# Optimization experiments

Measured on AMD Instinct MI355X. Metric: run time of the kernel, lower is better.

The kernel has to match this reference:

```python
import jax, jax.numpy as jnp
import numpy as np

DN = ('NCHW', 'OIHW', 'NCHW')


def dwconv(x, w, b, pad, dil=(1, 1)):
    # depthwise conv: w is (C, 1, kh, kw), feature_group_count = C
    y = jax.lax.conv_general_dilated(
        x, w, window_strides=(1, 1), padding=[pad[0], pad[1]],
        rhs_dilation=dil, dimension_numbers=DN, feature_group_count=w.shape[0])
    return y + b[None, :, None, None]


def setup_inputs() -> dict:
    key = jax.random.key(0)
    ks = jax.random.split(key, 18)
    dim, B, H, W = 512, 8, 64, 64
    s = 0.1  # keep depthwise chain numerically tame
    inp = {'x': jax.random.normal(ks[0], (B, dim, H, W), jnp.float32)}
    shapes = {
        'w0': (dim, 1, 5, 5), 'w0_1': (dim, 1, 1, 7), 'w0_2': (dim, 1, 7, 1),
        'w1_1': (dim, 1, 1, 11), 'w1_2': (dim, 1, 11, 1),
        'w2_1': (dim, 1, 1, 21), 'w2_2': (dim, 1, 21, 1),
        'w3': (dim, dim, 1, 1),
    }
    i = 1
    for name, shp in shapes.items():
        fan_in = shp[1] * shp[2] * shp[3]
        inp[name] = jax.random.normal(ks[i], shp, jnp.float32) * (s / np.sqrt(fan_in))
        inp['b' + name[1:]] = jax.random.normal(ks[i + 1], (dim,), jnp.float32) * 0.01
        i += 2
    return inp


def reference(x, w0, b0, w0_1, b0_1, w0_2, b0_2, w1_1, b1_1, w1_2, b1_2,
              w2_1, b2_1, w2_2, b2_2, w3, b3):
    u = x
    attn = dwconv(x, w0, b0, ((2, 2), (2, 2)))                       # 5x5 dw
    a0 = dwconv(attn, w0_1, b0_1, ((0, 0), (9, 9)), (3, 3))          # 1x7 d3
    a0 = dwconv(a0, w0_2, b0_2, ((9, 9), (0, 0)), (3, 3))            # 7x1 d3
    a1 = dwconv(attn, w1_1, b1_1, ((0, 0), (15, 15)), (3, 3))        # 1x11 d3
    a1 = dwconv(a1, w1_2, b1_2, ((15, 15), (0, 0)), (3, 3))          # 11x1 d3
    a2 = dwconv(attn, w2_1, b2_1, ((0, 0), (30, 30)), (3, 3))        # 1x21 d3
    a2 = dwconv(a2, w2_2, b2_2, ((30, 30), (0, 0)), (3, 3))          # 21x1 d3
    attn = attn + a0 + a1 + a2
    # 1x1 pointwise conv (dense channel mix)
    attn = jax.lax.conv_general_dilated(
        attn, w3, (1, 1), [(0, 0), (0, 0)], dimension_numbers=DN)
    attn = attn + b3[None, :, None, None]
    return attn * u
```

## Files before the change

### kernel.cpp

```cpp
#include <hip/hip_runtime.h>
#include <hip/hip_bf16.h>
#include <stdint.h>

typedef __attribute__((ext_vector_type(4))) float f32x4;
typedef __attribute__((ext_vector_type(8))) short s16x8;

#define XS_STRIDE 68
#define AS_STRIDE 132
#define AS_OFF 32
#define HT_STRIDE 68

__device__ static inline void load_lds_16B(const void* g, void* l) {
    __builtin_amdgcn_global_load_lds((const __attribute__((address_space(1))) void*)g,
                                     (__attribute__((address_space(3))) void*)l,
                                     16, 0, 0);
}


template<int K, int P, int P4>
__device__ __forceinline__ void branch_h(const float* __restrict__ wh, float bh,
                                         int r, int cq,
                                         const float* as_, float* ht_) {
    constexpr int SH = P4 - P;
    constexpr int NW = 16 + 2 * P;
    constexpr int NV = (NW + SH + 3) / 4;
    float vb[NV * 4];
    const float* src = as_ + r * AS_STRIDE + (AS_OFF - P4) + cq;
#pragma unroll
    for (int i = 0; i < NV; ++i) {
        f32x4 tmp = *(const f32x4*)(src + 4 * i);
        vb[4 * i + 0] = tmp[0]; vb[4 * i + 1] = tmp[1];
        vb[4 * i + 2] = tmp[2]; vb[4 * i + 3] = tmp[3];
    }
    float wr[K];
#pragma unroll
    for (int i = 0; i < K; ++i) wr[i] = wh[i];
    float out[16];
#pragma unroll
    for (int j = 0; j < 16; ++j) {
        float a = bh;
#pragma unroll
        for (int i = 0; i < K; ++i) a += vb[SH + j + 3 * i] * wr[i];
        out[j] = a;
    }
#pragma unroll
    for (int i = 0; i < 4; ++i) {
        f32x4 o = {out[4 * i], out[4 * i + 1], out[4 * i + 2], out[4 * i + 3]};
        *(f32x4*)(ht_ + r * HT_STRIDE + cq + 4 * i) = o;
    }
}

template<int K, int P>
__device__ __forceinline__ void branch_v(const float* __restrict__ wv, float bv,
                                         int cc, int r0,
                                         const float* ht_, float* ss) {
    constexpr int NW = 16 + 2 * P;
    float u[NW];
#pragma unroll
    for (int k = 0; k < NW; ++k) {
        int rr = r0 - P + k;
        u[k] = (rr >= 0 && rr < 64) ? ht_[rr * HT_STRIDE + cc] : 0.0f;
    }
    float wr[K];
#pragma unroll
    for (int i = 0; i < K; ++i) wr[i] = wv[i];
#pragma unroll
    for (int j = 0; j < 16; ++j) {
        float a = bv;
#pragma unroll
        for (int i = 0; i < K; ++i) a += u[j + 3 * i] * wr[i];
        ss[j] += a;
    }
}

__global__ __launch_bounds__(256, 2)
void k1_dw(const float* __restrict__ x,
           const float* __restrict__ w0,   const float* __restrict__ b0,
           const float* __restrict__ w0_1, const float* __restrict__ b0_1,
           const float* __restrict__ w0_2, const float* __restrict__ b0_2,
           const float* __restrict__ w1_1, const float* __restrict__ b1_1,
           const float* __restrict__ w1_2, const float* __restrict__ b1_2,
           const float* __restrict__ w2_1, const float* __restrict__ b2_1,
           const float* __restrict__ w2_2, const float* __restrict__ b2_2,
           __hip_bfloat16* __restrict__ s_out) {
    __shared__ float as[64 * AS_STRIDE];
    __shared__ float xs_ht[64 * XS_STRIDE];

    const int t = threadIdx.x;
    const int bid = blockIdx.x;
    const int c = bid & 511;
    const size_t pbase = (size_t)bid * 4096;

    {
        f32x4 z = {0.f, 0.f, 0.f, 0.f};
        f32x4* asv = (f32x4*)as;
#pragma unroll
        for (int i = 0; i < 9; ++i) {
            int idx = t + i * 256;
            if (idx < 64 * AS_STRIDE / 4) asv[idx] = z;
        }
        if (t < 64) {
            xs_ht[t * XS_STRIDE + 0] = 0.f; xs_ht[t * XS_STRIDE + 1] = 0.f;
            xs_ht[t * XS_STRIDE + 66] = 0.f; xs_ht[t * XS_STRIDE + 67] = 0.f;
        }
    }
    {
        const int r = t >> 2, cq = (t & 3) * 16;
        const f32x4* gx = (const f32x4*)(x + pbase + r * 64 + cq);
        f32x4* dst = (f32x4*)(xs_ht + r * XS_STRIDE + 2 + cq);
#pragma unroll
        for (int i = 0; i < 4; ++i) dst[i] = gx[i];
    }
    __syncthreads();

    {
        const int r = t >> 2, cq = (t & 3) * 16;
        const float bias = b0[c];
        float acc[16];
#pragma unroll
        for (int j = 0; j < 16; ++j) acc[j] = bias;
        const float* wc = w0 + c * 25;
#pragma unroll
        for (int dr = 0; dr < 5; ++dr) {
            int rr = r + dr - 2;
            if (rr >= 0 && rr <= 63) {
                float v[20];
                const float* src = xs_ht + rr * XS_STRIDE + cq;
#pragma unroll
                for (int i = 0; i < 5; ++i) {
                    f32x4 tmp = *(const f32x4*)(src + 4 * i);
                    v[4 * i + 0] = tmp[0]; v[4 * i + 1] = tmp[1];
                    v[4 * i + 2] = tmp[2]; v[4 * i + 3] = tmp[3];
                }
                const float* wrow = wc + dr * 5;
#pragma unroll
                for (int j = 0; j < 16; ++j)
#pragma unroll
                    for (int dc = 0; dc < 5; ++dc)
                        acc[j] += v[j + dc] * wrow[dc];
            }
        }
#pragma unroll
        for (int i = 0; i < 4; ++i) {
            f32x4 o = {acc[4 * i], acc[4 * i + 1], acc[4 * i + 2], acc[4 * i + 3]};
            *(f32x4*)(as + r * AS_STRIDE + AS_OFF + cq + 4 * i) = o;
        }
    }
    __syncthreads();

    const int r = t >> 2, cq = (t & 3) * 16;
    const int cc = t & 63, r0 = (t >> 6) * 16;

    float ss[16];
#pragma unroll
    for (int j = 0; j < 16; ++j) ss[j] = as[(r0 + j) * AS_STRIDE + AS_OFF + cc];

    branch_h<7, 9, 12>(w0_1 + c * 7, b0_1[c], r, cq, as, xs_ht);
    __syncthreads();
    branch_v<7, 9>(w0_2 + c * 7, b0_2[c], cc, r0, xs_ht, ss);
    __syncthreads();
    branch_h<11, 15, 16>(w1_1 + c * 11, b1_1[c], r, cq, as, xs_ht);
    __syncthreads();
    branch_v<11, 15>(w1_2 + c * 11, b1_2[c], cc, r0, xs_ht, ss);
    __syncthreads();
    branch_h<21, 30, 32>(w2_1 + c * 21, b2_1[c], r, cq, as, xs_ht);
    __syncthreads();
    branch_v<21, 30>(w2_2 + c * 21, b2_2[c], cc, r0, xs_ht, ss);

#pragma unroll
    for (int j = 0; j < 16; ++j)
        s_out[pbase + (size_t)(r0 + j) * 64 + cc] = __float2bfloat16(ss[j]);
}

__global__ __launch_bounds__(256, 4)
void k2_transpose(const __hip_bfloat16* __restrict__ s_px,
                  __hip_bfloat16* __restrict__ st) {
    __shared__ short tile[64][66];
    const int b = blockIdx.x;
    const int n = b >> 9, rem = b & 511;
    const int cib = rem >> 6, pxb = rem & 63;
    const int t = threadIdx.x;

    {
        const int row = t >> 2, chunk = (t & 3) * 16;
        const __hip_bfloat16* src =
            s_px + ((size_t)(n * 512 + cib * 64 + row)) * 4096 + pxb * 64 + chunk;
        s16x8 v0 = *(const s16x8*)(src);
        s16x8 v1 = *(const s16x8*)(src + 8);
#pragma unroll
        for (int k = 0; k < 8; ++k) {
            tile[row][chunk + k] = v0[k];
            tile[row][chunk + 8 + k] = v1[k];
        }
    }
    __syncthreads();
    {
        const int pxl = t >> 2, cich = (t & 3) * 16;
        s16x8 o0, o1;
#pragma unroll
        for (int k = 0; k < 8; ++k) {
            o0[k] = tile[cich + k][pxl];
            o1[k] = tile[cich + 8 + k][pxl];
        }
        __hip_bfloat16* dst =
            st + ((size_t)(n * 4096 + pxb * 64 + pxl)) * 512 + cib * 64 + cich;
        *(s16x8*)dst = o0;
        *(s16x8*)(dst + 8) = o1;
    }
}

__global__ __launch_bounds__(256, 4)
void k2b_cast(const float* __restrict__ w3, __hip_bfloat16* __restrict__ w3b) {
    const int i = (blockIdx.x * 256 + threadIdx.x) * 4;
    f32x4 v = *(const f32x4*)(w3 + i);
    union { __hip_bfloat16 h[4]; uint32_t u[2]; } pk;
#pragma unroll
    for (int k = 0; k < 4; ++k) pk.h[k] = __float2bfloat16(v[k]);
    *(uint32_t*)((char*)(w3b + i)) = pk.u[0];
    *(uint32_t*)((char*)(w3b + i) + 4) = pk.u[1];
}

__global__ __launch_bounds__(256, 2)
void k3_gemm(const __hip_bfloat16* __restrict__ w3b,
             const __hip_bfloat16* __restrict__ st,
             const float* __restrict__ b3,
             const float* __restrict__ x,
             float* __restrict__ out) {
    __shared__ __hip_bfloat16 As[128 * 64];
    __shared__ __hip_bfloat16 Bs[128 * 64];

    const int t = threadIdx.x;
    const int lane = t & 63, wv = t >> 6;
    const int waveM = wv & 1, waveN = wv >> 1;
    const int coBase = blockIdx.x * 128;
    const int nb = blockIdx.y;
    const int n = nb >> 5, pxTile = nb & 31;
    const int pxBase = pxTile * 128;
    const int lr = lane & 15, lq = lane >> 4;

    f32x4 acc[4][4] = {};

    for (int k0 = 0; k0 < 512; k0 += 64) {
#pragma unroll
        for (int s = 0; s < 4; ++s) {
            const int seg = wv * 4 + s;
            const int rowg = seg * 8 + (lane >> 3);
            const int kcol = k0 + (lane & 7) * 8;
            const __hip_bfloat16* ga = w3b + (size_t)(coBase + rowg) * 512 + kcol;
            load_lds_16B(ga, &As[seg * 512]);
            const __hip_bfloat16* gb =
                st + ((size_t)(n * 4096 + pxBase + rowg)) * 512 + kcol;
            load_lds_16B(gb, &Bs[seg * 512]);
        }
        __syncthreads();
#pragma unroll
        for (int kk = 0; kk < 64; kk += 32) {
            s16x8 af[4], bf[4];
#pragma unroll
            for (int m = 0; m < 4; ++m)
                af[m] = *(const s16x8*)&As[(waveM * 64 + m * 16 + lr) * 64 + kk + lq * 8];
#pragma unroll
            for (int nn = 0; nn < 4; ++nn)
                bf[nn] = *(const s16x8*)&Bs[(waveN * 64 + nn * 16 + lr) * 64 + kk + lq * 8];
#pragma unroll
            for (int m = 0; m < 4; ++m)
#pragma unroll
                for (int nn = 0; nn < 4; ++nn)
                    acc[m][nn] = __builtin_amdgcn_mfma_f32_16x16x32_bf16(
                        af[m], bf[nn], acc[m][nn], 0, 0, 0);
        }
        __syncthreads();
    }

#pragma unroll
    for (int m = 0; m < 4; ++m) {
#pragma unroll
        for (int nn = 0; nn < 4; ++nn) {
            const int px = pxBase + waveN * 64 + nn * 16 + lr;
#pragma unroll
            for (int j = 0; j < 4; ++j) {
                const int co = coBase + waveM * 64 + m * 16 + lq * 4 + j;
                const size_t idx = ((size_t)(n * 512 + co)) * 4096 + px;
                out[idx] = (acc[m][nn][j] + b3[co]) * x[idx];
            }
        }
    }
}

extern "C" void kernel_launch(void* const* d_in, const int* in_sizes, int n_in,
                              void* d_out, int out_size, void* d_ws, size_t ws_size,
                              hipStream_t stream) {
    (void)in_sizes; (void)n_in; (void)out_size; (void)ws_size;
    const float* x    = (const float*)d_in[0];
    const float* w0   = (const float*)d_in[1];
    const float* b0   = (const float*)d_in[2];
    const float* w0_1 = (const float*)d_in[3];
    const float* b0_1 = (const float*)d_in[4];
    const float* w0_2 = (const float*)d_in[5];
    const float* b0_2 = (const float*)d_in[6];
    const float* w1_1 = (const float*)d_in[7];
    const float* b1_1 = (const float*)d_in[8];
    const float* w1_2 = (const float*)d_in[9];
    const float* b1_2 = (const float*)d_in[10];
    const float* w2_1 = (const float*)d_in[11];
    const float* b2_1 = (const float*)d_in[12];
    const float* w2_2 = (const float*)d_in[13];
    const float* b2_2 = (const float*)d_in[14];
    const float* w3   = (const float*)d_in[15];
    const float* b3   = (const float*)d_in[16];
    float* out = (float*)d_out;

    __hip_bfloat16* s_px = (__hip_bfloat16*)d_out;
    __hip_bfloat16* st   = (__hip_bfloat16*)d_ws;
    __hip_bfloat16* w3b  = (__hip_bfloat16*)((char*)d_ws + ((size_t)32 << 20));

    k1_dw<<<4096, 256, 0, stream>>>(x, w0, b0, w0_1, b0_1, w0_2, b0_2,
                                    w1_1, b1_1, w1_2, b1_2, w2_1, b2_1,
                                    w2_2, b2_2, s_px);
    k2_transpose<<<4096, 256, 0, stream>>>(s_px, st);
    k2b_cast<<<256, 256, 0, stream>>>(w3, w3b);
    k3_gemm<<<dim3(4, 256), 256, 0, stream>>>(w3b, st, b3, x, out);
}
```

Before: 273.0 us.

## Store 5x5 depthwise output in bf16 LDS and double-buffer GEMM K tiles

```diff
diff --git a/kernel.cpp b/kernel.cpp
--- a/kernel.cpp
+++ b/kernel.cpp
@@ -16,25 +16,34 @@
                                      16, 0, 0);
 }
 
-
-template<int K, int P, int P4>
+__device__ static inline float b2f(short u) {
+    return __uint_as_float(((unsigned int)(unsigned short)u) << 16);
+}
+__device__ static inline short f2b(float f) {
+    __hip_bfloat16 b = __float2bfloat16(f);
+    return *reinterpret_cast<short*>(&b);
+}
+
+
+template<int K, int P>
 __device__ __forceinline__ void branch_h(const float* __restrict__ wh, float bh,
                                          int r, int cq,
-                                         const float* as_, float* ht_) {
-    constexpr int SH = P4 - P;
+                                         const __hip_bfloat16* as_, float* ht_) {
     constexpr int NW = 16 + 2 * P;
-    constexpr int NV = (NW + SH + 3) / 4;
-    float vb[NV * 4];
-    const float* src = as_ + r * AS_STRIDE + (AS_OFF - P4) + cq;
-#pragma unroll
-    for (int i = 0; i < NV; ++i) {
-        f32x4 tmp = *(const f32x4*)(src + 4 * i);
-        vb[4 * i + 0] = tmp[0]; vb[4 * i + 1] = tmp[1];
-        vb[4 * i + 2] = tmp[2]; vb[4 * i + 3] = tmp[3];
-    }
+    constexpr int SH = (AS_OFF - P) & 7;
+    constexpr int START = AS_OFF - P - SH;
+    constexpr int NV = (SH + NW + 7) / 8;
     float wr[K];
 #pragma unroll
     for (int i = 0; i < K; ++i) wr[i] = wh[i];
+    float vb[NV * 8];
+    const __hip_bfloat16* src = as_ + r * AS_STRIDE + START + cq;
+#pragma unroll
+    for (int v = 0; v < NV; ++v) {
+        s16x8 q = *(const s16x8*)(src + 8 * v);
+#pragma unroll
+        for (int e = 0; e < 8; ++e) vb[8 * v + e] = b2f(q[e]);
+    }
     float out[16];
 #pragma unroll
     for (int j = 0; j < 16; ++j) {
@@ -83,7 +92,7 @@
            const float* __restrict__ w2_1, const float* __restrict__ b2_1,
            const float* __restrict__ w2_2, const float* __restrict__ b2_2,
            __hip_bfloat16* __restrict__ s_out) {
-    __shared__ float as[64 * AS_STRIDE];
+    __shared__ __hip_bfloat16 as[64 * AS_STRIDE];
     __shared__ float xs_ht[64 * XS_STRIDE];
 
     const int t = threadIdx.x;
@@ -92,12 +101,12 @@
     const size_t pbase = (size_t)bid * 4096;
 
     {
-        f32x4 z = {0.f, 0.f, 0.f, 0.f};
-        f32x4* asv = (f32x4*)as;
-#pragma unroll
-        for (int i = 0; i < 9; ++i) {
+        s16x8 z = {0, 0, 0, 0, 0, 0, 0, 0};
+        s16x8* asv = (s16x8*)as;
+#pragma unroll
+        for (int i = 0; i < 5; ++i) {
             int idx = t + i * 256;
-            if (idx < 64 * AS_STRIDE / 4) asv[idx] = z;
+            if (idx < 64 * AS_STRIDE / 8) asv[idx] = z;
         }
         if (t < 64) {
             xs_ht[t * XS_STRIDE + 0] = 0.f; xs_ht[t * XS_STRIDE + 1] = 0.f;
@@ -141,9 +150,11 @@
             }
         }
 #pragma unroll
-        for (int i = 0; i < 4; ++i) {
-            f32x4 o = {acc[4 * i], acc[4 * i + 1], acc[4 * i + 2], acc[4 * i + 3]};
-            *(f32x4*)(as + r * AS_STRIDE + AS_OFF + cq + 4 * i) = o;
+        for (int i = 0; i < 2; ++i) {
+            s16x8 o;
+#pragma unroll
+            for (int e = 0; e < 8; ++e) o[e] = f2b(acc[i * 8 + e]);
+            *(s16x8*)(as + r * AS_STRIDE + AS_OFF + cq + i * 8) = o;
         }
     }
     __syncthreads();
@@ -153,17 +164,18 @@
 
     float ss[16];
 #pragma unroll
-    for (int j = 0; j < 16; ++j) ss[j] = as[(r0 + j) * AS_STRIDE + AS_OFF + cc];
-
-    branch_h<7, 9, 12>(w0_1 + c * 7, b0_1[c], r, cq, as, xs_ht);
+    for (int j = 0; j < 16; ++j)
+        ss[j] = b2f(*reinterpret_cast<const short*>(&as[(r0 + j) * AS_STRIDE + AS_OFF + cc]));
+
+    branch_h<7, 9>(w0_1 + c * 7, b0_1[c], r, cq, as, xs_ht);
     __syncthreads();
     branch_v<7, 9>(w0_2 + c * 7, b0_2[c], cc, r0, xs_ht, ss);
     __syncthreads();
-    branch_h<11, 15, 16>(w1_1 + c * 11, b1_1[c], r, cq, as, xs_ht);
+    branch_h<11, 15>(w1_1 + c * 11, b1_1[c], r, cq, as, xs_ht);
     __syncthreads();
     branch_v<11, 15>(w1_2 + c * 11, b1_2[c], cc, r0, xs_ht, ss);
     __syncthreads();
-    branch_h<21, 30, 32>(w2_1 + c * 21, b2_1[c], r, cq, as, xs_ht);
+    branch_h<21, 30>(w2_1 + c * 21, b2_1[c], r, cq, as, xs_ht);
     __syncthreads();
     branch_v<21, 30>(w2_2 + c * 21, b2_2[c], cc, r0, xs_ht, ss);
 
@@ -226,8 +238,8 @@
              const float* __restrict__ b3,
              const float* __restrict__ x,
              float* __restrict__ out) {
-    __shared__ __hip_bfloat16 As[128 * 64];
-    __shared__ __hip_bfloat16 Bs[128 * 64];
+    __shared__ __hip_bfloat16 As[2][128 * 64];
+    __shared__ __hip_bfloat16 Bs[2][128 * 64];
 
     const int t = threadIdx.x;
     const int lane = t & 63, wv = t >> 6;
@@ -238,30 +250,38 @@
     const int pxBase = pxTile * 128;
     const int lr = lane & 15, lq = lane >> 4;
 
-    f32x4 acc[4][4] = {};
-
-    for (int k0 = 0; k0 < 512; k0 += 64) {
+    const int rowg = (lane >> 3);
+    const int kLane = (lane & 7) * 8;
+
+    auto stage = [&](int b, int k0) {
 #pragma unroll
         for (int s = 0; s < 4; ++s) {
             const int seg = wv * 4 + s;
-            const int rowg = seg * 8 + (lane >> 3);
-            const int kcol = k0 + (lane & 7) * 8;
-            const __hip_bfloat16* ga = w3b + (size_t)(coBase + rowg) * 512 + kcol;
-            load_lds_16B(ga, &As[seg * 512]);
-            const __hip_bfloat16* gb =
-                st + ((size_t)(n * 4096 + pxBase + rowg)) * 512 + kcol;
-            load_lds_16B(gb, &Bs[seg * 512]);
-        }
-        __syncthreads();
+            const int row = seg * 8 + rowg;
+            const int kcol = k0 + kLane;
+            load_lds_16B(w3b + (size_t)(coBase + row) * 512 + kcol, &As[b][seg * 512]);
+            load_lds_16B(st + ((size_t)(n * 4096 + pxBase + row)) * 512 + kcol,
+                         &Bs[b][seg * 512]);
+        }
+    };
+
+    f32x4 acc[4][4] = {};
+
+    stage(0, 0);
+    __syncthreads();
+
+    int cur = 0;
+    for (int it = 0; it < 8; ++it) {
+        if (it < 7) stage(cur ^ 1, (it + 1) * 64);
 #pragma unroll
         for (int kk = 0; kk < 64; kk += 32) {
             s16x8 af[4], bf[4];
 #pragma unroll
             for (int m = 0; m < 4; ++m)
-                af[m] = *(const s16x8*)&As[(waveM * 64 + m * 16 + lr) * 64 + kk + lq * 8];
+                af[m] = *(const s16x8*)&As[cur][(waveM * 64 + m * 16 + lr) * 64 + kk + lq * 8];
 #pragma unroll
             for (int nn = 0; nn < 4; ++nn)
-                bf[nn] = *(const s16x8*)&Bs[(waveN * 64 + nn * 16 + lr) * 64 + kk + lq * 8];
+                bf[nn] = *(const s16x8*)&Bs[cur][(waveN * 64 + nn * 16 + lr) * 64 + kk + lq * 8];
 #pragma unroll
             for (int m = 0; m < 4; ++m)
 #pragma unroll
@@ -269,7 +289,8 @@
                     acc[m][nn] = __builtin_amdgcn_mfma_f32_16x16x32_bf16(
                         af[m], bf[nn], acc[m][nn], 0, 0, 0);
         }
-        __syncthreads();
+        if (it < 7) __syncthreads();
+        cur ^= 1;
     }
 
 #pragma unroll
```

Result: slower. 297.2 us (+8.8%).
